# Kernel tuning notes

Hardware: AMD Instinct MI355X
Metric: run time of the kernel (lower is better)

Reference implementation:

```python
import jax, jax.numpy as jnp
import numpy as np

WIN = 25            # window size (win_h == win_w == 25)
DIM = 256           # channels
DIM_HEAD = 32
HEADS = DIM // DIM_HEAD   # 8
HIDDEN = int(DIM * 2.0)   # mlp_ratio = 2.0
EPS = 1e-5


def _rel_pos_indices(w=WIN):
    # replicates the buffer built in Attention.__init__
    pos = np.arange(w)
    gi, gj = np.meshgrid(pos, pos, indexing='ij')
    grid = np.stack([gi.ravel(), gj.ravel()], axis=-1)          # (w*w, 2)
    rel = grid[:, None, :] - grid[None, :, :] + (w - 1)          # (n, n, 2)
    return jnp.asarray(rel[..., 0] * (2 * w - 1) + rel[..., 1])  # (n, n) int


def setup_inputs() -> dict:
    key = jax.random.key(0)
    ks = jax.random.split(key, 8)
    s = 0.02
    d = DIM
    return {
        'x': jax.random.normal(ks[0], (2, d, 100, 100), jnp.float32),
        'w_qkv': jax.random.normal(ks[1], (3 * d, d), jnp.float32) * s,
        'w_out': jax.random.normal(ks[2], (d, d), jnp.float32) * s,
        'rel_bias_table': jax.random.normal(ks[3], ((2 * WIN - 1) ** 2, HEADS), jnp.float32) * s,
        'gamma2': jnp.ones((d,), jnp.float32),
        'beta2': jnp.zeros((d,), jnp.float32),
        'w1': jax.random.normal(ks[4], (HIDDEN, d), jnp.float32) * s,
        'b1': jnp.zeros((HIDDEN,), jnp.float32),
        'w2': jax.random.normal(ks[5], (d, HIDDEN), jnp.float32) * s,
        'b2': jnp.zeros((d,), jnp.float32),
    }


def _layernorm(x, g, b, eps=EPS):
    m = x.mean(-1, keepdims=True)
    v = ((x - m) ** 2).mean(-1, keepdims=True)
    return (x - m) / jnp.sqrt(v + eps) * g + b


def reference(x, w_qkv, w_out, rel_bias_table, gamma2, beta2, w1, b1, w2, b2):
    b, d, H, W = x.shape
    nh, nw = H // WIN, W // WIN
    h, dh = HEADS, DIM_HEAD
    scale = dh ** -0.5
    n = WIN * WIN

    # --- window partition: (b, d, H, W) -> (b*nh*nw, n, d) ---
    xw = x.reshape(b, d, nh, WIN, nw, WIN).transpose(0, 2, 4, 3, 5, 1)
    xw = xw.reshape(b * nh * nw, n, d)

    # --- windowed attention with relative-position bias (norm1 unused in source) ---
    qkv = xw @ w_qkv.T                         # (B, n, 3d)
    q, k, v = jnp.split(qkv, 3, axis=-1)
    split_heads = lambda t: t.reshape(t.shape[0], n, h, dh).transpose(0, 2, 1, 3)
    q = split_heads(q) * scale                 # (B, h, n, dh)
    k = split_heads(k)
    v = split_heads(v)

    sim = jnp.einsum('bhid,bhjd->bhij', q, k)  # (B, h, n, n)
    bias = rel_bias_table[_rel_pos_indices()]  # (n, n, h)
    sim = sim + bias.transpose(2, 0, 1)[None]
    attn = jax.nn.softmax(sim, axis=-1)
    out = jnp.einsum('bhij,bhjd->bhid', attn, v)            # (B, h, n, dh)
    out = out.transpose(0, 2, 1, 3).reshape(-1, n, d)        # head-major concat: (m d)
    out = out @ w_out.T                                      # (B, n, d)

    # --- un-partition: (b*nh*nw, n, d) -> (b, d, H, W) ---
    xa = out.reshape(b, nh, nw, WIN, WIN, d).transpose(0, 5, 1, 3, 2, 4)
    xa = xa.reshape(b, d, H, W)

    # --- norm2 + MLP + residual ---
    y = xa.transpose(0, 2, 3, 1).reshape(b, H * W, d)
    y = _layernorm(y, gamma2, beta2)
    y = jax.nn.gelu(y @ w1.T + b1, approximate=False) @ w2.T + b2
    y = y.reshape(b, H, W, d).transpose(0, 3, 1, 2)
    return x + y
```

## Files before the change

### kernel.cpp

```cpp
#include <hip/hip_runtime.h>


using f32x4 = __attribute__((ext_vector_type(4))) float;
using s16x8 = __attribute__((ext_vector_type(8))) short;
using u32x4 = __attribute__((ext_vector_type(4))) unsigned;

__device__ __forceinline__ ushort f2b(float f) {
  union { float f; unsigned u; } v; v.f = f;
  return (ushort)((v.u + 0x7FFFu + ((v.u >> 16) & 1u)) >> 16);
}
__device__ __forceinline__ ushort f2b_fast(float f) {
  union { float f; unsigned u; } v; v.f = f;
  return (ushort)((v.u + 0x8000u) >> 16);
}
__device__ __forceinline__ float b2f(ushort u) {
  union { unsigned u; float f; } v; v.u = ((unsigned)u) << 16; return v.f;
}
__device__ __forceinline__ float lo2f(unsigned w) {
  union { unsigned u; float f; } v; v.u = w << 16; return v.f;
}
__device__ __forceinline__ float hi2f(unsigned w) {
  union { unsigned u; float f; } v; v.u = w & 0xffff0000u; return v.f;
}

__device__ __forceinline__ unsigned cvtpk(float lo, float hi) {
  unsigned r;
  asm("v_cvt_pk_bf16_f32 %0, %1, %2" : "=v"(r) : "v"(lo), "v"(hi));
  return r;
}
__device__ __forceinline__ void pl32(unsigned& a, unsigned& b) {
  asm("v_permlane32_swap_b32 %0, %1" : "+v"(a), "+v"(b));
}
__device__ __forceinline__ void pl16(unsigned& a, unsigned& b) {
  asm("v_permlane16_swap_b32 %0, %1" : "+v"(a), "+v"(b));
}

__device__ __forceinline__ void gld16(const void* g, void* l) {
  __builtin_amdgcn_global_load_lds((const __attribute__((address_space(1))) void*)g,
                                   (__attribute__((address_space(3))) void*)l, 16, 0, 0);
}

template<int KB>
__device__ __forceinline__ void gemm_core(const ushort* __restrict__ A, int lda,
                                          const ushort* __restrict__ B, int ldb,
                                          f32x4 acc[4][4]) {
  __shared__ ushort As[128 * 64];
  __shared__ ushort Bs[128 * 64];
  const int tid = threadIdx.x;
  const int lane = tid & 63;
  const int wv = tid >> 6;
  const int wr = (wv >> 1) * 64;
  const int wc = (wv & 1) * 64;
  const int srow = (lane >> 3);
  const int sg = ((lane & 7) ^ (srow & 7)) * 8;
  f32x4 zero = {0.f, 0.f, 0.f, 0.f};
#pragma unroll
  for (int mt = 0; mt < 4; ++mt)
#pragma unroll
    for (int nt = 0; nt < 4; ++nt) acc[mt][nt] = zero;

  for (int kb = 0; kb < KB; ++kb) {
#pragma unroll
    for (int j = 0; j < 4; ++j) {
      int r0 = wv * 32 + j * 8;
      int row = r0 + srow;
      gld16(A + row * lda + kb * 64 + sg, &As[r0 * 64]);
      gld16(B + row * ldb + kb * 64 + sg, &Bs[r0 * 64]);
    }
    __syncthreads();
#pragma unroll
    for (int ks = 0; ks < 2; ++ks) {
      s16x8 af[4], bfr[4];
      const int G = ks * 4 + (lane >> 4);
#pragma unroll
      for (int mt = 0; mt < 4; ++mt) {
        int row = wr + mt * 16 + (lane & 15);
        af[mt] = *(const s16x8*)&As[row * 64 + (G ^ (row & 7)) * 8];
      }
#pragma unroll
      for (int nt = 0; nt < 4; ++nt) {
        int row = wc + nt * 16 + (lane & 15);
        bfr[nt] = *(const s16x8*)&Bs[row * 64 + (G ^ (row & 7)) * 8];
      }
#pragma unroll
      for (int mt = 0; mt < 4; ++mt)
#pragma unroll
        for (int nt = 0; nt < 4; ++nt)
          acc[mt][nt] = __builtin_amdgcn_mfma_f32_16x16x32_bf16(af[mt], bfr[nt], acc[mt][nt], 0, 0, 0);
    }
    __syncthreads();
  }
}

__global__ __launch_bounds__(256) void k_prep(const float* __restrict__ x,
                                              const float* __restrict__ wqkv,
                                              const float* __restrict__ wout,
                                              const float* __restrict__ w1,
                                              const float* __restrict__ w2,
                                              const float* __restrict__ table,
                                              ushort* __restrict__ Xw,
                                              ushort* __restrict__ wqkvb,
                                              ushort* __restrict__ woutb,
                                              ushort* __restrict__ w1b,
                                              ushort* __restrict__ w2b,
                                              ushort* __restrict__ biasPh) {
  __shared__ ushort smem[64 * 264];
  const int bid = blockIdx.x, tid = threadIdx.x;
  if (bid < 320) {
    ushort (*Ls)[264] = (ushort(*)[264])smem;
    const int t0 = bid * 64;
    const int w = t0 / 640;
    const int tokbase = t0 - w * 640;
    const int b = w >> 4, wh = (w >> 2) & 3, ww = w & 3;
    for (int i = tid; i < 64 * 256; i += 256) {
      int c = i >> 6, tl = i & 63;
      int tok = tokbase + tl;
      ushort val = 0;
      if (tok < 625) {
        int ii = tok / 25, jj = tok - ii * 25;
        val = f2b(x[((b * 256 + c) * 100 + wh * 25 + ii) * 100 + ww * 25 + jj]);
      }
      Ls[tl][c] = val;
    }
    __syncthreads();
    for (int i = tid; i < 64 * 32; i += 256) {
      int tl = i >> 5, g = (i & 31) * 8;
      *(uint4*)(Xw + (t0 + tl) * 256 + g) = *(const uint4*)&Ls[tl][g];
    }
  } else if (bid < 832) {
    int v = (bid - 320) * 1024 + tid * 4;
    const float* src; ushort* dst; int off;
    if (v < 196608)      { src = wqkv; dst = wqkvb; off = v; }
    else if (v < 262144) { src = wout; dst = woutb; off = v - 196608; }
    else if (v < 393216) { src = w1;   dst = w1b;   off = v - 262144; }
    else                 { src = w2;   dst = w2b;   off = v - 393216; }
    float4 f = *(const float4*)(src + off);
    ushort4 u; u.x = f2b(f.x); u.y = f2b(f.y); u.z = f2b(f.z); u.w = f2b(f.w);
    *(ushort4*)(dst + off) = u;
  } else {
    float* tl = (float*)smem;
    const int qb = bid - 832;
    const int h = qb / 40, t = qb - (qb / 40) * 40;
    for (int i = tid; i < 2401; i += 256) tl[i] = table[i * 8 + h] * 1.4426950408889634f;
    __syncthreads();
    const int lane = tid >> 2, rr = tid & 3;
    const int quad = lane >> 4, cl = lane & 15;
    int qrow = t * 16 + cl;
    int qg = (qrow < 625) ? qrow : 0;
    const int ri = qg / 25, ci = qg - ri * 25;
    for (int cc = 0; cc < 4; ++cc)
      for (int cp = 0; cp < 5; ++cp)
#pragma unroll
        for (int codd = 0; codd < 2; ++codd) {
          int kv = cc * 160 + (cp * 2 + codd) * 16 + quad * 4 + rr;
          float v = -1e30f;
          if (kv < 625) {
            int rj = kv / 25, cj = kv - rj * 25;
            v = tl[(ri - rj + 24) * 49 + (ci - cj + 24)];
          }
          biasPh[((((h * 40 + t) * 4 + cc) * 5 + cp) * 64 + lane) * 8 + codd * 4 + rr] = f2b(v);
        }
  }
}

__global__ __launch_bounds__(256) void k_qkv(const ushort* __restrict__ Xw,
                                             const ushort* __restrict__ Wb,
                                             ushort* __restrict__ Qb,
                                             ushort* __restrict__ Kb,
                                             ushort* __restrict__ VbT) {
  f32x4 acc[4][4];
  gemm_core<4>(Xw + blockIdx.x * 128 * 256, 256, Wb + blockIdx.y * 128 * 256, 256, acc);
  const int lane = threadIdx.x & 63, wv = threadIdx.x >> 6;
  const int wr = (wv >> 1) * 64, wc = (wv & 1) * 64;
  const int which = blockIdx.y >> 1;
  const float QSC = 0.17677669529663687f * 1.4426950408889634f;
#pragma unroll
  for (int mt = 0; mt < 4; ++mt) {
#pragma unroll
    for (int nt = 0; nt < 4; ++nt) {
      int n = blockIdx.y * 128 + wc + nt * 16 + (lane & 15);
      int h = (n >> 5) & 7, ch = n & 31;
      int m0 = blockIdx.x * 128 + wr + mt * 16 + (lane >> 4) * 4;
      int w = m0 / 640, tok0 = m0 - w * 640;
      if (which == 2) {
        ushort4 pk;
        pk.x = f2b_fast(acc[mt][nt][0]); pk.y = f2b_fast(acc[mt][nt][1]);
        pk.z = f2b_fast(acc[mt][nt][2]); pk.w = f2b_fast(acc[mt][nt][3]);
        *(ushort4*)(VbT + (((w << 3) + h) * 32 + ch) * 640 + tok0) = pk;
      } else {
        ushort* dst = which == 0 ? Qb : Kb;
        float sc = which == 0 ? QSC : 1.f;
#pragma unroll
        for (int r = 0; r < 4; ++r)
          dst[(((w << 3) + h) * 640 + tok0 + r) * 32 + ch] = f2b_fast(acc[mt][nt][r] * sc);
      }
    }
  }
}

__global__ __launch_bounds__(256, 4) void k_attn(const ushort* __restrict__ Qb,
                                                 const ushort* __restrict__ Kb,
                                                 const ushort* __restrict__ VbT,
                                                 const ushort* __restrict__ biasPh,
                                                 ushort* __restrict__ AO) {
  const int tid = threadIdx.x;
  const int lane = tid & 63;
  const int wv = tid >> 6;
  const int quad = lane >> 4;
  const int cl = lane & 15;
  const int bid = blockIdx.x;
  const int h = bid & 7;
  const int rem = bid >> 3;
  const int win = rem / 5;
  const int tg = rem - win * 5;
  const ushort* Qg = Qb + (win * 8 + h) * 20480;
  const ushort* Kg = Kb + (win * 8 + h) * 20480;
  const ushort* Vt = VbT + (win * 8 + h) * 20480;

  const int t0 = tg * 8 + wv * 2;
  const s16x8 qf0 = *(const s16x8*)(Qg + (t0 * 16 + cl) * 32 + quad * 8);
  const s16x8 qf1 = *(const s16x8*)(Qg + ((t0 + 1) * 16 + cl) * 32 + quad * 8);
  s16x8 ones;
#pragma unroll
  for (int j = 0; j < 8; ++j) ones[j] = (short)0x3F80;

  const f32x4 zero = {0.f, 0.f, 0.f, 0.f};
  f32x4 o00 = zero, o01 = zero, o10 = zero, o11 = zero;
  f32x4 sum0 = zero, sum1 = zero;

  const ushort* bp0 = biasPh + ((h * 40 + t0) * 20) * 512 + lane * 8;

#pragma unroll
  for (int cc = 0; cc < 4; ++cc) {
#pragma unroll
    for (int kc = 0; kc < 5; ++kc) {
      const s16x8 kfA = *(const s16x8*)(Kg + (cc * 160 + (2 * kc) * 16 + cl) * 32 + quad * 8);
      const s16x8 kfB = *(const s16x8*)(Kg + (cc * 160 + (2 * kc + 1) * 16 + cl) * 32 + quad * 8);
      const s16x8 vfa = *(const s16x8*)(Vt + cl * 640 + cc * 160 + kc * 32 + quad * 8);
      const s16x8 vfb = *(const s16x8*)(Vt + (16 + cl) * 640 + cc * 160 + kc * 32 + quad * 8);
#pragma unroll
      for (int tlp = 0; tlp < 2; ++tlp) {
        const s16x8 qf = tlp ? qf1 : qf0;
        s16x8 bb = *(const s16x8*)(bp0 + (tlp * 20 + cc * 5 + kc) * 512);
        const unsigned* bw = (const unsigned*)&bb;
        f32x4 c0, c1;
        c0[0] = lo2f(bw[0]); c0[1] = hi2f(bw[0]); c0[2] = lo2f(bw[1]); c0[3] = hi2f(bw[1]);
        c1[0] = lo2f(bw[2]); c1[1] = hi2f(bw[2]); c1[2] = lo2f(bw[3]); c1[3] = hi2f(bw[3]);
        f32x4 s0 = __builtin_amdgcn_mfma_f32_16x16x32_bf16(kfA, qf, c0, 0, 0, 0);
        f32x4 s1 = __builtin_amdgcn_mfma_f32_16x16x32_bf16(kfB, qf, c1, 0, 0, 0);
#pragma unroll
        for (int r = 0; r < 4; ++r) {
          s0[r] = __builtin_amdgcn_exp2f(s0[r]);
          s1[r] = __builtin_amdgcn_exp2f(s1[r]);
        }
        unsigned a0 = cvtpk(s0[0], s0[1]);
        unsigned a1 = cvtpk(s0[2], s0[3]);
        unsigned b0 = cvtpk(s1[0], s1[1]);
        unsigned b1 = cvtpk(s1[2], s1[3]);
        pl32(a0, b0); pl16(a0, b0);
        pl32(a1, b1); pl16(a1, b1);
        u32x4 pw; pw[0] = a0; pw[1] = a1; pw[2] = b0; pw[3] = b1;
        s16x8 pf = __builtin_bit_cast(s16x8, pw);
        f32x4& o0 = tlp ? o10 : o00;
        f32x4& o1 = tlp ? o11 : o01;
        f32x4& sm = tlp ? sum1 : sum0;
        o0 = __builtin_amdgcn_mfma_f32_16x16x32_bf16(vfa, pf, o0, 0, 0, 0);
        o1 = __builtin_amdgcn_mfma_f32_16x16x32_bf16(vfb, pf, o1, 0, 0, 0);
        sm = __builtin_amdgcn_mfma_f32_16x16x32_bf16(ones, pf, sm, 0, 0, 0);
      }
    }
  }
#pragma unroll
  for (int tlp = 0; tlp < 2; ++tlp) {
    const f32x4& o0 = tlp ? o10 : o00;
    const f32x4& o1 = tlp ? o11 : o01;
    const f32x4& sm = tlp ? sum1 : sum0;
    int tok = (t0 + tlp) * 16 + cl;
    if (tok < 625) {
      float inv = 1.f / sm[0];
      int base = (win * 640 + tok) * 256 + h * 32 + quad * 4;
      ushort4 p0, p1;
      p0.x = f2b_fast(o0[0] * inv); p0.y = f2b_fast(o0[1] * inv);
      p0.z = f2b_fast(o0[2] * inv); p0.w = f2b_fast(o0[3] * inv);
      p1.x = f2b_fast(o1[0] * inv); p1.y = f2b_fast(o1[1] * inv);
      p1.z = f2b_fast(o1[2] * inv); p1.w = f2b_fast(o1[3] * inv);
      *(ushort4*)(AO + base) = p0;
      *(ushort4*)(AO + base + 16) = p1;
    }
  }
}

__global__ __launch_bounds__(256, 2) void k_out_ln(const ushort* __restrict__ AO,
                                                   const ushort* __restrict__ Wb,
                                                   const float* __restrict__ gamma,
                                                   const float* __restrict__ beta,
                                                   ushort* __restrict__ Yn) {
  __shared__ ushort As[64 * 64];
  __shared__ ushort Bs[256 * 64];
  __shared__ float red[2][64][2];
  const int tid = threadIdx.x;
  const int lane = tid & 63;
  const int wv = tid >> 6;
  const int wr = (wv >> 1) * 32, wc = (wv & 1) * 128;
  const int quad = lane >> 4, cl = lane & 15;
  const int srow = lane >> 3;
  const int sg = ((lane & 7) ^ (srow & 7)) * 8;
  f32x4 zero = {0.f, 0.f, 0.f, 0.f};
  f32x4 acc[2][8];
#pragma unroll
  for (int mt = 0; mt < 2; ++mt)
#pragma unroll
    for (int nt = 0; nt < 8; ++nt) acc[mt][nt] = zero;

  const ushort* A = AO + blockIdx.x * 64 * 256;
  for (int kb = 0; kb < 4; ++kb) {
#pragma unroll
    for (int i = 0; i < 10; ++i) {
      int r0 = (wv + i * 4) * 8;
      int row = r0 + srow;
      if (r0 < 64) gld16(A + row * 256 + kb * 64 + sg, &As[r0 * 64]);
      else         gld16(Wb + (row - 64) * 256 + kb * 64 + sg, &Bs[(r0 - 64) * 64]);
    }
    __syncthreads();
#pragma unroll
    for (int ks = 0; ks < 2; ++ks) {
      s16x8 af[2], bfr[8];
      const int G = ks * 4 + quad;
#pragma unroll
      for (int mt = 0; mt < 2; ++mt) {
        int row = wr + mt * 16 + cl;
        af[mt] = *(const s16x8*)&As[row * 64 + (G ^ (row & 7)) * 8];
      }
#pragma unroll
      for (int nt = 0; nt < 8; ++nt) {
        int row = wc + nt * 16 + cl;
        bfr[nt] = *(const s16x8*)&Bs[row * 64 + (G ^ (row & 7)) * 8];
      }
#pragma unroll
      for (int mt = 0; mt < 2; ++mt)
#pragma unroll
        for (int nt = 0; nt < 8; ++nt)
          acc[mt][nt] = __builtin_amdgcn_mfma_f32_16x16x32_bf16(af[mt], bfr[nt], acc[mt][nt], 0, 0, 0);
    }
    __syncthreads();
  }
#pragma unroll
  for (int mt = 0; mt < 2; ++mt)
#pragma unroll
    for (int r = 0; r < 4; ++r) {
      float s = 0.f, ss = 0.f;
#pragma unroll
      for (int nt = 0; nt < 8; ++nt) { float v = acc[mt][nt][r]; s += v; ss += v * v; }
      s += __shfl_xor(s, 1, 64); ss += __shfl_xor(ss, 1, 64);
      s += __shfl_xor(s, 2, 64); ss += __shfl_xor(ss, 2, 64);
      s += __shfl_xor(s, 4, 64); ss += __shfl_xor(ss, 4, 64);
      s += __shfl_xor(s, 8, 64); ss += __shfl_xor(ss, 8, 64);
      if (cl == 0) {
        int row = wr + mt * 16 + quad * 4 + r;
        red[wc >> 7][row][0] = s;
        red[wc >> 7][row][1] = ss;
      }
    }
  __syncthreads();
  float g[8], bt[8];
#pragma unroll
  for (int nt = 0; nt < 8; ++nt) { int n = wc + nt * 16 + cl; g[nt] = gamma[n]; bt[nt] = beta[n]; }
  const int m0 = blockIdx.x * 64;
#pragma unroll
  for (int mt = 0; mt < 2; ++mt)
#pragma unroll
    for (int r = 0; r < 4; ++r) {
      int row = wr + mt * 16 + quad * 4 + r;
      int m = m0 + row;
      int w = m / 640, tok = m - w * 640;
      if (tok < 625) {
        float sum = red[0][row][0] + red[1][row][0];
        float ssum = red[0][row][1] + red[1][row][1];
        float mean = sum * 0.00390625f;
        float var = ssum * 0.00390625f - mean * mean;
        float rstd = rsqrtf(var + 1e-5f);
        int b = w >> 4, whh = (w >> 2) & 3, www = w & 3;
        int ii = tok / 25, jj = tok - ii * 25;
        int p = (whh * 25 + ii) * 100 + www * 25 + jj;
        ushort* dst = Yn + (b * 10000 + p) * 256;
#pragma unroll
        for (int nt = 0; nt < 8; ++nt) {
          float v = (acc[mt][nt][r] - mean) * rstd * g[nt] + bt[nt];
          dst[wc + nt * 16 + cl] = f2b_fast(v);
        }
      }
    }
}

__global__ __launch_bounds__(256) void k_fc1(const ushort* __restrict__ Yn,
                                             const ushort* __restrict__ W1b,
                                             const float* __restrict__ b1,
                                             ushort* __restrict__ G) {
  f32x4 acc[4][4];
  gemm_core<4>(Yn + blockIdx.x * 128 * 256, 256, W1b + blockIdx.y * 128 * 256, 256, acc);
  const int lane = threadIdx.x & 63, wv = threadIdx.x >> 6;
  const int wr = (wv >> 1) * 64, wc = (wv & 1) * 64;
#pragma unroll
  for (int mt = 0; mt < 4; ++mt)
#pragma unroll
    for (int nt = 0; nt < 4; ++nt) {
      int n = blockIdx.y * 128 + wc + nt * 16 + (lane & 15);
      float bias = b1[n];
#pragma unroll
      for (int r = 0; r < 4; ++r) {
        int m = blockIdx.x * 128 + wr + mt * 16 + (lane >> 4) * 4 + r;
        float v = acc[mt][nt][r] + bias;
        v = 0.5f * v * (1.f + erff(v * 0.70710678118f));
        G[m * 512 + n] = f2b_fast(v);
      }
    }
}

__global__ __launch_bounds__(256) void k_fc2(const ushort* __restrict__ W2b,
                                             const ushort* __restrict__ G,
                                             const float* __restrict__ b2,
                                             const float* __restrict__ x,
                                             float* __restrict__ out) {
  f32x4 acc[4][4];
  gemm_core<8>(W2b + blockIdx.x * 128 * 512, 512, G + blockIdx.y * 128 * 512, 512, acc);
  const int lane = threadIdx.x & 63, wv = threadIdx.x >> 6;
  const int wr = (wv >> 1) * 64, wc = (wv & 1) * 64;
#pragma unroll
  for (int mt = 0; mt < 4; ++mt)
#pragma unroll
    for (int nt = 0; nt < 4; ++nt) {
      int t = blockIdx.y * 128 + wc + nt * 16 + (lane & 15);
      if (t < 20000) {
        int b = t / 10000, p = t - b * 10000;
#pragma unroll
        for (int r = 0; r < 4; ++r) {
          int c = blockIdx.x * 128 + wr + mt * 16 + (lane >> 4) * 4 + r;
          int idx = (b * 256 + c) * 10000 + p;
          out[idx] = x[idx] + acc[mt][nt][r] + b2[c];
        }
      }
    }
}

extern "C" void kernel_launch(void* const* d_in, const int* in_sizes, int n_in,
                              void* d_out, int out_size, void* d_ws, size_t ws_size,
                              hipStream_t stream) {
  const float* x     = (const float*)d_in[0];
  const float* wqkv  = (const float*)d_in[1];
  const float* wout  = (const float*)d_in[2];
  const float* bias  = (const float*)d_in[3];
  const float* gamma = (const float*)d_in[4];
  const float* beta  = (const float*)d_in[5];
  const float* w1    = (const float*)d_in[6];
  const float* b1    = (const float*)d_in[7];
  const float* w2    = (const float*)d_in[8];
  const float* b2    = (const float*)d_in[9];
  float* out = (float*)d_out;
  char* ws = (char*)d_ws;

  ushort* Xw    = (ushort*)(ws + 0);
  ushort* AO    = Xw;
  ushort* wqkvb = (ushort*)(ws + 10485760);
  ushort* woutb = (ushort*)(ws + 10878976);
  ushort* w1b   = (ushort*)(ws + 11010048);
  ushort* w2b   = (ushort*)(ws + 11272192);
  ushort* Qb    = (ushort*)(ws + 11534336);
  ushort* Kb    = (ushort*)(ws + 22020096);
  ushort* VbT   = (ushort*)(ws + 32505856);
  ushort* biasPh= (ushort*)(ws + 42991616);
  ushort* Yn    = (ushort*)(ws + 22020096);
  ushort* G     = (ushort*)(ws + 32505856);

  k_prep  <<<1152, 256, 0, stream>>>(x, wqkv, wout, w1, w2, bias,
                                     Xw, wqkvb, woutb, w1b, w2b, biasPh);
  k_qkv   <<<dim3(160, 6), 256, 0, stream>>>(Xw, wqkvb, Qb, Kb, VbT);
  k_attn  <<<1280, 256, 0, stream>>>(Qb, Kb, VbT, biasPh, AO);
  k_out_ln<<<320, 256, 0, stream>>>(AO, woutb, gamma, beta, Yn);
  k_fc1   <<<dim3(157, 4), 256, 0, stream>>>(Yn, w1b, b1, G);
  k_fc2   <<<dim3(2, 157), 256, 0, stream>>>(w2b, G, b2, x, out);
}
```

Before: 223.5 us.

## Give each attention wave four query tiles and replace ones-MFMA row sum with shuffles

The attention kernel now runs 128-thread blocks where each wave handles four 16-token query tiles instead of two. Each K/V fragment load is therefore reused across twice as many queries, and keys are processed in 64-key chunks with a sched_barrier after the loads. The softmax denominator is now accumulated in scalar registers and reduced with lane permutes at the end, replacing the extra MFMA against a ones vector. This cuts K/V global loads and MFMA count, at the cost of higher register pressure, lower occupancy (launch bounds 128,3) and a non-unrolled outer loop.

After: 208.4 us. 1.07x faster.

```diff
diff --git a/kernel.cpp b/kernel.cpp
--- a/kernel.cpp
+++ b/kernel.cpp
@@ -198,7 +198,7 @@
   }
 }
 
-__global__ __launch_bounds__(256, 4) void k_attn(const ushort* __restrict__ Qb,
+__global__ __launch_bounds__(128, 3) void k_attn(const ushort* __restrict__ Qb,
                                                  const ushort* __restrict__ Kb,
                                                  const ushort* __restrict__ VbT,
                                                  const ushort* __restrict__ biasPh,
@@ -217,73 +217,95 @@
   const ushort* Kg = Kb + (win * 8 + h) * 20480;
   const ushort* Vt = VbT + (win * 8 + h) * 20480;
 
-  const int t0 = tg * 8 + wv * 2;
-  const s16x8 qf0 = *(const s16x8*)(Qg + (t0 * 16 + cl) * 32 + quad * 8);
-  const s16x8 qf1 = *(const s16x8*)(Qg + ((t0 + 1) * 16 + cl) * 32 + quad * 8);
-  s16x8 ones;
-#pragma unroll
-  for (int j = 0; j < 8; ++j) ones[j] = (short)0x3F80;
+  const int t0 = tg * 8 + wv * 4;
+  s16x8 qf[4];
+#pragma unroll
+  for (int tlp = 0; tlp < 4; ++tlp)
+    qf[tlp] = *(const s16x8*)(Qg + ((t0 + tlp) * 16 + cl) * 32 + quad * 8);
 
   const f32x4 zero = {0.f, 0.f, 0.f, 0.f};
-  f32x4 o00 = zero, o01 = zero, o10 = zero, o11 = zero;
-  f32x4 sum0 = zero, sum1 = zero;
-
-  const ushort* bp0 = biasPh + ((h * 40 + t0) * 20) * 512 + lane * 8;
-
-#pragma unroll
-  for (int cc = 0; cc < 4; ++cc) {
-#pragma unroll
-    for (int kc = 0; kc < 5; ++kc) {
-      const s16x8 kfA = *(const s16x8*)(Kg + (cc * 160 + (2 * kc) * 16 + cl) * 32 + quad * 8);
-      const s16x8 kfB = *(const s16x8*)(Kg + (cc * 160 + (2 * kc + 1) * 16 + cl) * 32 + quad * 8);
-      const s16x8 vfa = *(const s16x8*)(Vt + cl * 640 + cc * 160 + kc * 32 + quad * 8);
-      const s16x8 vfb = *(const s16x8*)(Vt + (16 + cl) * 640 + cc * 160 + kc * 32 + quad * 8);
-#pragma unroll
-      for (int tlp = 0; tlp < 2; ++tlp) {
-        const s16x8 qf = tlp ? qf1 : qf0;
-        s16x8 bb = *(const s16x8*)(bp0 + (tlp * 20 + cc * 5 + kc) * 512);
-        const unsigned* bw = (const unsigned*)&bb;
-        f32x4 c0, c1;
-        c0[0] = lo2f(bw[0]); c0[1] = hi2f(bw[0]); c0[2] = lo2f(bw[1]); c0[3] = hi2f(bw[1]);
-        c1[0] = lo2f(bw[2]); c1[1] = hi2f(bw[2]); c1[2] = lo2f(bw[3]); c1[3] = hi2f(bw[3]);
-        f32x4 s0 = __builtin_amdgcn_mfma_f32_16x16x32_bf16(kfA, qf, c0, 0, 0, 0);
-        f32x4 s1 = __builtin_amdgcn_mfma_f32_16x16x32_bf16(kfB, qf, c1, 0, 0, 0);
-#pragma unroll
-        for (int r = 0; r < 4; ++r) {
-          s0[r] = __builtin_amdgcn_exp2f(s0[r]);
-          s1[r] = __builtin_amdgcn_exp2f(s1[r]);
-        }
-        unsigned a0 = cvtpk(s0[0], s0[1]);
-        unsigned a1 = cvtpk(s0[2], s0[3]);
-        unsigned b0 = cvtpk(s1[0], s1[1]);
-        unsigned b1 = cvtpk(s1[2], s1[3]);
-        pl32(a0, b0); pl16(a0, b0);
-        pl32(a1, b1); pl16(a1, b1);
-        u32x4 pw; pw[0] = a0; pw[1] = a1; pw[2] = b0; pw[3] = b1;
-        s16x8 pf = __builtin_bit_cast(s16x8, pw);
-        f32x4& o0 = tlp ? o10 : o00;
-        f32x4& o1 = tlp ? o11 : o01;
-        f32x4& sm = tlp ? sum1 : sum0;
-        o0 = __builtin_amdgcn_mfma_f32_16x16x32_bf16(vfa, pf, o0, 0, 0, 0);
-        o1 = __builtin_amdgcn_mfma_f32_16x16x32_bf16(vfb, pf, o1, 0, 0, 0);
-        sm = __builtin_amdgcn_mfma_f32_16x16x32_bf16(ones, pf, sm, 0, 0, 0);
-      }
+  f32x4 o0[4], o1[4];
+  float ssum[4];
+#pragma unroll
+  for (int tlp = 0; tlp < 4; ++tlp) { o0[tlp] = zero; o1[tlp] = zero; ssum[tlp] = 0.f; }
+
+  const ushort* bpB = biasPh + ((h * 40 + t0) * 20) * 512 + lane * 8;
+
+  for (int ch2 = 0; ch2 < 10; ++ch2) {
+    s16x8 kf[4], va[2], vb[2];
+#pragma unroll
+    for (int j = 0; j < 4; ++j)
+      kf[j] = *(const s16x8*)(Kg + (ch2 * 64 + j * 16 + cl) * 32 + quad * 8);
+#pragma unroll
+    for (int j = 0; j < 2; ++j) {
+      va[j] = *(const s16x8*)(Vt + cl * 640 + ch2 * 64 + j * 32 + quad * 8);
+      vb[j] = *(const s16x8*)(Vt + (16 + cl) * 640 + ch2 * 64 + j * 32 + quad * 8);
+    }
+    __builtin_amdgcn_sched_barrier(0);
+#pragma unroll
+    for (int tlp = 0; tlp < 4; ++tlp) {
+      const s16x8 bb0 = *(const s16x8*)(bpB + (tlp * 20 + 2 * ch2) * 512);
+      const s16x8 bb1 = *(const s16x8*)(bpB + (tlp * 20 + 2 * ch2 + 1) * 512);
+      const unsigned* w0 = (const unsigned*)&bb0;
+      const unsigned* w1 = (const unsigned*)&bb1;
+      f32x4 s0, s1, s2, s3;
+      s0[0] = lo2f(w0[0]); s0[1] = hi2f(w0[0]); s0[2] = lo2f(w0[1]); s0[3] = hi2f(w0[1]);
+      s1[0] = lo2f(w0[2]); s1[1] = hi2f(w0[2]); s1[2] = lo2f(w0[3]); s1[3] = hi2f(w0[3]);
+      s2[0] = lo2f(w1[0]); s2[1] = hi2f(w1[0]); s2[2] = lo2f(w1[1]); s2[3] = hi2f(w1[1]);
+      s3[0] = lo2f(w1[2]); s3[1] = hi2f(w1[2]); s3[2] = lo2f(w1[3]); s3[3] = hi2f(w1[3]);
+      s0 = __builtin_amdgcn_mfma_f32_16x16x32_bf16(kf[0], qf[tlp], s0, 0, 0, 0);
+      s1 = __builtin_amdgcn_mfma_f32_16x16x32_bf16(kf[1], qf[tlp], s1, 0, 0, 0);
+      s2 = __builtin_amdgcn_mfma_f32_16x16x32_bf16(kf[2], qf[tlp], s2, 0, 0, 0);
+      s3 = __builtin_amdgcn_mfma_f32_16x16x32_bf16(kf[3], qf[tlp], s3, 0, 0, 0);
+#pragma unroll
+      for (int r = 0; r < 4; ++r) {
+        s0[r] = __builtin_amdgcn_exp2f(s0[r]);
+        s1[r] = __builtin_amdgcn_exp2f(s1[r]);
+        s2[r] = __builtin_amdgcn_exp2f(s2[r]);
+        s3[r] = __builtin_amdgcn_exp2f(s3[r]);
+      }
+      ssum[tlp] += ((s0[0] + s0[1]) + (s0[2] + s0[3])) + ((s1[0] + s1[1]) + (s1[2] + s1[3]))
+                 + ((s2[0] + s2[1]) + (s2[2] + s2[3])) + ((s3[0] + s3[1]) + (s3[2] + s3[3]));
+      unsigned a0 = cvtpk(s0[0], s0[1]);
+      unsigned a1 = cvtpk(s0[2], s0[3]);
+      unsigned b0 = cvtpk(s1[0], s1[1]);
+      unsigned b1 = cvtpk(s1[2], s1[3]);
+      pl32(a0, b0); pl16(a0, b0);
+      pl32(a1, b1); pl16(a1, b1);
+      u32x4 pw0; pw0[0] = a0; pw0[1] = a1; pw0[2] = b0; pw0[3] = b1;
+      s16x8 pf0 = __builtin_bit_cast(s16x8, pw0);
+      o0[tlp] = __builtin_amdgcn_mfma_f32_16x16x32_bf16(va[0], pf0, o0[tlp], 0, 0, 0);
+      o1[tlp] = __builtin_amdgcn_mfma_f32_16x16x32_bf16(vb[0], pf0, o1[tlp], 0, 0, 0);
+      unsigned a2 = cvtpk(s2[0], s2[1]);
+      unsigned a3 = cvtpk(s2[2], s2[3]);
+      unsigned b2 = cvtpk(s3[0], s3[1]);
+      unsigned b3 = cvtpk(s3[2], s3[3]);
+      pl32(a2, b2); pl16(a2, b2);
+      pl32(a3, b3); pl16(a3, b3);
+      u32x4 pw1; pw1[0] = a2; pw1[1] = a3; pw1[2] = b2; pw1[3] = b3;
+      s16x8 pf1 = __builtin_bit_cast(s16x8, pw1);
+      o0[tlp] = __builtin_amdgcn_mfma_f32_16x16x32_bf16(va[1], pf1, o0[tlp], 0, 0, 0);
+      o1[tlp] = __builtin_amdgcn_mfma_f32_16x16x32_bf16(vb[1], pf1, o1[tlp], 0, 0, 0);
     }
   }
 #pragma unroll
-  for (int tlp = 0; tlp < 2; ++tlp) {
-    const f32x4& o0 = tlp ? o10 : o00;
-    const f32x4& o1 = tlp ? o11 : o01;
-    const f32x4& sm = tlp ? sum1 : sum0;
+  for (int tlp = 0; tlp < 4; ++tlp) {
+    float s = ssum[tlp];
+    unsigned ua = __builtin_bit_cast(unsigned, s), ub = ua;
+    pl32(ua, ub);
+    s = __builtin_bit_cast(float, ua) + __builtin_bit_cast(float, ub);
+    ua = __builtin_bit_cast(unsigned, s); ub = ua;
+    pl16(ua, ub);
+    s = __builtin_bit_cast(float, ua) + __builtin_bit_cast(float, ub);
     int tok = (t0 + tlp) * 16 + cl;
     if (tok < 625) {
-      float inv = 1.f / sm[0];
+      float inv = 1.f / s;
       int base = (win * 640 + tok) * 256 + h * 32 + quad * 4;
       ushort4 p0, p1;
-      p0.x = f2b_fast(o0[0] * inv); p0.y = f2b_fast(o0[1] * inv);
-      p0.z = f2b_fast(o0[2] * inv); p0.w = f2b_fast(o0[3] * inv);
-      p1.x = f2b_fast(o1[0] * inv); p1.y = f2b_fast(o1[1] * inv);
-      p1.z = f2b_fast(o1[2] * inv); p1.w = f2b_fast(o1[3] * inv);
+      p0.x = f2b_fast(o0[tlp][0] * inv); p0.y = f2b_fast(o0[tlp][1] * inv);
+      p0.z = f2b_fast(o0[tlp][2] * inv); p0.w = f2b_fast(o0[tlp][3] * inv);
+      p1.x = f2b_fast(o1[tlp][0] * inv); p1.y = f2b_fast(o1[tlp][1] * inv);
+      p1.z = f2b_fast(o1[tlp][2] * inv); p1.w = f2b_fast(o1[tlp][3] * inv);
       *(ushort4*)(AO + base) = p0;
       *(ushort4*)(AO + base + 16) = p1;
     }
@@ -474,7 +496,7 @@
   k_prep  <<<1152, 256, 0, stream>>>(x, wqkv, wout, w1, w2, bias,
                                      Xw, wqkvb, woutb, w1b, w2b, biasPh);
   k_qkv   <<<dim3(160, 6), 256, 0, stream>>>(Xw, wqkvb, Qb, Kb, VbT);
-  k_attn  <<<1280, 256, 0, stream>>>(Qb, Kb, VbT, biasPh, AO);
+  k_attn  <<<1280, 128, 0, stream>>>(Qb, Kb, VbT, biasPh, AO);
   k_out_ln<<<320, 256, 0, stream>>>(AO, woutb, gamma, beta, Yn);
   k_fc1   <<<dim3(157, 4), 256, 0, stream>>>(Yn, w1b, b1, G);
   k_fc2   <<<dim3(2, 157), 256, 0, stream>>>(w2b, G, b2, x, out);
```
